# Kernel optimization log

Hardware: AMD Instinct MI355X
Metric: run time of the kernel (lower is better)

Reference implementation:

```python
import jax, jax.numpy as jnp
import numpy as np

N_HEAD = 16


def setup_inputs() -> dict:
    key = jax.random.key(0)
    ks = jax.random.split(key, 9)
    d = 1024
    s = 0.02
    return {
        "x": jax.random.normal(ks[0], (8, 448, d), jnp.float32),
        "xa": jax.random.normal(ks[1], (8, 1500, d), jnp.float32),
        "Wq": jax.random.normal(ks[2], (d, d), jnp.float32) * s,
        "bq": jax.random.normal(ks[3], (d,), jnp.float32) * s,
        "Wk": jax.random.normal(ks[4], (d, d), jnp.float32) * s,
        "Wv": jax.random.normal(ks[5], (d, d), jnp.float32) * s,
        "bv": jax.random.normal(ks[6], (d,), jnp.float32) * s,
        "Wo": jax.random.normal(ks[7], (d, d), jnp.float32) * s,
        "bo": jax.random.normal(ks[8], (d,), jnp.float32) * s,
    }


def reference(x, xa, Wq, bq, Wk, Wv, bv, Wo, bo):
    B, T, D = x.shape
    S = xa.shape[1]
    H = N_HEAD
    Dh = D // H
    scale = Dh ** -0.25  # applied to both q and k, as in the original

    q = x @ Wq + bq            # [B,T,D]
    k = xa @ Wk                # [B,S,D] (no bias)
    v = xa @ Wv + bv           # [B,S,D]

    q = q.reshape(B, T, H, Dh) * scale
    k = k.reshape(B, S, H, Dh) * scale
    v = v.reshape(B, S, H, Dh)

    qk = jnp.einsum("bthd,bshd->bhts", q, k).astype(jnp.float32)  # pre-softmax logits
    w = jax.nn.softmax(qk, axis=-1).astype(q.dtype)
    wv = jnp.einsum("bhts,bshd->bthd", w, v).reshape(B, T, D)

    out = wv @ Wo + bo
    return out, qk
```

## Files before the change

### kernel.cpp

```cpp
#include <hip/hip_runtime.h>
#include <hip/hip_bf16.h>
#include <cstdint>
#include <cstddef>

typedef __bf16  bf16x8  __attribute__((ext_vector_type(8)));
typedef float   f32x4   __attribute__((ext_vector_type(4)));
typedef ushort  ushort8 __attribute__((ext_vector_type(8)));

#define ASYNC16(gp, lp)                                                        \
  __builtin_amdgcn_global_load_lds(                                            \
      (const __attribute__((address_space(1))) void*)(gp),                     \
      (__attribute__((address_space(3))) void*)(lp), 16, 0, 0)

__device__ __forceinline__ ushort f2bf(float f) {
  __hip_bfloat16 h = __float2bfloat16(f);
  ushort u; __builtin_memcpy(&u, &h, 2); return u;
}

#define SINF (-1e30f)

__global__ __launch_bounds__(256) void to_bf16(
    const float* __restrict__ src, ushort* __restrict__ dst, int n8) {
  int i = blockIdx.x * 256 + threadIdx.x;
  const int stride = gridDim.x * 256;
  for (; i < n8; i += stride) {
    const float4* s = (const float4*)(src + (size_t)i * 8);
    float4 a0 = s[0], a1 = s[1];
    ushort8 u = { f2bf(a0.x), f2bf(a0.y), f2bf(a0.z), f2bf(a0.w),
                  f2bf(a1.x), f2bf(a1.y), f2bf(a1.z), f2bf(a1.w) };
    *(ushort8*)&dst[(size_t)i * 8] = u;
  }
}

__global__ __launch_bounds__(256) void transpose_w(
    const float* __restrict__ W0, const float* __restrict__ W1,
    const float* __restrict__ W2, const float* __restrict__ W3,
    ushort* __restrict__ out) {
  __shared__ float tile[32][33];
  const float* W = blockIdx.z == 0 ? W0 : blockIdx.z == 1 ? W1
                 : blockIdx.z == 2 ? W2 : W3;
  ushort* T = out + (size_t)blockIdx.z * (1024u * 1024u);
  const int n0 = blockIdx.x * 32, k0 = blockIdx.y * 32;
  const int t = threadIdx.x;
  const int r = t >> 3, c = (t & 7) * 4;
  float4 v = *(const float4*)&W[(size_t)(k0 + r) * 1024 + n0 + c];
  tile[r][c + 0] = v.x; tile[r][c + 1] = v.y;
  tile[r][c + 2] = v.z; tile[r][c + 3] = v.w;
  __syncthreads();
  ushort4 o;
  o.x = f2bf(tile[c + 0][r]); o.y = f2bf(tile[c + 1][r]);
  o.z = f2bf(tile[c + 2][r]); o.w = f2bf(tile[c + 3][r]);
  *(ushort4*)&T[(size_t)(n0 + r) * 1024 + k0 + c] = o;
}

__global__ __launch_bounds__(256) void transpose_v(
    const ushort* __restrict__ v_s, ushort* __restrict__ v_t) {
  __shared__ ushort tile[32][36];
  const int bh = blockIdx.z;
  const int b = bh >> 4, h = bh & 15;
  const int d0 = blockIdx.y * 32;
  const int s0 = blockIdx.x * 32;
  const int t = threadIdx.x;
  const int r = t >> 3, c4 = (t & 7) * 4;
  const int s = s0 + r;
  ushort4 v = {0, 0, 0, 0};
  if (s < 1500)
    v = *(const ushort4*)&v_s[(size_t)(b * 1500 + s) * 1024 + h * 64 + d0 + c4];
  tile[r][c4 + 0] = v.x; tile[r][c4 + 1] = v.y;
  tile[r][c4 + 2] = v.z; tile[r][c4 + 3] = v.w;
  __syncthreads();
  ushort4 o;
  o.x = tile[c4 + 0][r]; o.y = tile[c4 + 1][r];
  o.z = tile[c4 + 2][r]; o.w = tile[c4 + 3][r];
  *(ushort4*)&v_t[((size_t)bh * 64 + d0 + r) * 1536 + s0 + c4] = o;
}

template <bool A_F32, bool C_F32>
__global__ __launch_bounds__(256) void gemm_bt(
    const void* __restrict__ Ap, const ushort* __restrict__ Bt,
    const float* __restrict__ bias, void* __restrict__ Cp,
    int M, float scale) {
  __shared__ ushort As[128 * 32];
  __shared__ ushort Bs[128 * 32];
  const int tid  = threadIdx.x;
  const int lane = tid & 63, w = tid >> 6;
  const int m15  = lane & 15, q4 = lane >> 4;
  const int wm   = w >> 1,  wn = w & 1;
  const int m0 = blockIdx.x * 128, n0 = blockIdx.y * 128;
  const int sr = lane >> 2;
  const int sc = (lane & 3) * 8;
  f32x4 acc[4][4] = {};
  for (int k0 = 0; k0 < 1024; k0 += 32) {
    __syncthreads();
    #pragma unroll
    for (int j = 0; j < 2; ++j) {
      int n = w * 2 + j;
      int r = n * 16 + sr;
      ASYNC16(&Bt[(size_t)(n0 + r) * 1024 + k0 + sc], &Bs[n * 512]);
    }
    if constexpr (A_F32) {
      const float* Af = (const float*)Ap;
      #pragma unroll
      for (int h = 0; h < 2; ++h) {
        int g = tid + h * 256;
        int row = g >> 2, kg = g & 3;
        int ga = min(m0 + row, M - 1);
        const float* src = &Af[(size_t)ga * 1024 + k0 + kg * 8];
        float4 a0 = *(const float4*)src;
        float4 a1 = *(const float4*)(src + 4);
        ushort8 u = { f2bf(a0.x), f2bf(a0.y), f2bf(a0.z), f2bf(a0.w),
                      f2bf(a1.x), f2bf(a1.y), f2bf(a1.z), f2bf(a1.w) };
        *(ushort8*)&As[row * 32 + kg * 8] = u;
      }
    } else {
      const ushort* Ab = (const ushort*)Ap;
      #pragma unroll
      for (int j = 0; j < 2; ++j) {
        int n = w * 2 + j;
        int r = n * 16 + sr;
        int ga = min(m0 + r, M - 1);
        ASYNC16(&Ab[(size_t)ga * 1024 + k0 + sc], &As[n * 512]);
      }
    }
    __syncthreads();
    bf16x8 af[4], bfr[4];
    #pragma unroll
    for (int i = 0; i < 4; ++i)
      af[i] = *(const bf16x8*)&As[(wm * 64 + i * 16 + m15) * 32 + q4 * 8];
    #pragma unroll
    for (int i = 0; i < 4; ++i)
      bfr[i] = *(const bf16x8*)&Bs[(wn * 64 + i * 16 + m15) * 32 + q4 * 8];
    #pragma unroll
    for (int i = 0; i < 4; ++i)
      #pragma unroll
      for (int j = 0; j < 4; ++j)
        acc[i][j] = __builtin_amdgcn_mfma_f32_16x16x32_bf16(af[i], bfr[j],
                                                            acc[i][j], 0, 0, 0);
  }
  #pragma unroll
  for (int j = 0; j < 4; ++j) {
    int col = n0 + wn * 64 + j * 16 + m15;
    float bb = bias ? bias[col] : 0.f;
    #pragma unroll
    for (int i = 0; i < 4; ++i) {
      #pragma unroll
      for (int r = 0; r < 4; ++r) {
        int row = m0 + wm * 64 + i * 16 + q4 * 4 + r;
        if (row < M) {
          float v = (acc[i][j][r] + bb) * scale;
          if constexpr (C_F32)
            ((float*)Cp)[(size_t)row * 1024 + col] = v;
          else
            ((ushort*)Cp)[(size_t)row * 1024 + col] = f2bf(v);
        }
      }
    }
  }
}

__global__ __launch_bounds__(256) void attn(
    const ushort* __restrict__ q_s, const ushort* __restrict__ k_s,
    const ushort* __restrict__ v_t, float* __restrict__ qk_out,
    ushort* __restrict__ wv) {
  __shared__ ushort Kb[64 * 64];
  __shared__ ushort Pw[4][16 * 72];
  const int tid  = threadIdx.x;
  const int lane = tid & 63, w = tid >> 6;
  const int m15  = lane & 15, q4 = lane >> 4;
  const int h = blockIdx.y, b = blockIdx.z;
  const int t0 = blockIdx.x * 64;
  const int trow = t0 + w * 16;
  const ushort* qrow = &q_s[(size_t)(b * 448 + trow + m15) * 1024 + h * 64];
  bf16x8 qf0 = *(const bf16x8*)&qrow[q4 * 8];
  bf16x8 qf1 = *(const bf16x8*)&qrow[32 + q4 * 8];
  f32x4 o[4] = {};
  float m_r[4] = {SINF, SINF, SINF, SINF};
  float l_r[4] = {0.f, 0.f, 0.f, 0.f};
  const int krb = lane >> 3;
  const int kc_sw = (((lane & 7) ^ krb) * 8);
  const ushort* vbase =
      &v_t[((size_t)(b * 16 + h) * 64 + m15) * 1536 + q4 * 8];
  for (int s0 = 0; s0 < 1500; s0 += 64) {
    __syncthreads();
    #pragma unroll
    for (int j = 0; j < 2; ++j) {
      int n = w * 2 + j;
      int sg = min(s0 + n * 8 + krb, 1499);
      ASYNC16(&k_s[(size_t)(b * 1500 + sg) * 1024 + h * 64 + kc_sw],
              &Kb[n * 512]);
    }
    __syncthreads();
    f32x4 lg[4];
    #pragma unroll
    for (int scol = 0; scol < 4; ++scol) {
      const int r = scol * 16 + m15;
      const int sw = (m15 & 7) * 8;
      bf16x8 kf0 = *(const bf16x8*)&Kb[r * 64 + ((q4 * 8) ^ sw)];
      bf16x8 kf1 = *(const bf16x8*)&Kb[r * 64 + ((32 + q4 * 8) ^ sw)];
      f32x4 a = {};
      a = __builtin_amdgcn_mfma_f32_16x16x32_bf16(qf0, kf0, a, 0, 0, 0);
      a = __builtin_amdgcn_mfma_f32_16x16x32_bf16(qf1, kf1, a, 0, 0, 0);
      lg[scol] = a;
    }
    float mc[4] = {SINF, SINF, SINF, SINF};
    #pragma unroll
    for (int scol = 0; scol < 4; ++scol) {
      bool valid = (s0 + scol * 16 + m15) < 1500;
      #pragma unroll
      for (int r = 0; r < 4; ++r)
        mc[r] = fmaxf(mc[r], valid ? lg[scol][r] : SINF);
    }
    #pragma unroll
    for (int off = 1; off < 16; off <<= 1)
      #pragma unroll
      for (int r = 0; r < 4; ++r)
        mc[r] = fmaxf(mc[r], __shfl_xor(mc[r], off));
    #pragma unroll
    for (int r = 0; r < 4; ++r) {
      float mn = fmaxf(m_r[r], mc[r]);
      float alpha = __expf(m_r[r] - mn);
      l_r[r] *= alpha;
      #pragma unroll
      for (int d = 0; d < 4; ++d) o[d][r] *= alpha;
      m_r[r] = mn;
    }
    float psum[4] = {0.f, 0.f, 0.f, 0.f};
    #pragma unroll
    for (int scol = 0; scol < 4; ++scol) {
      int sg = s0 + scol * 16 + m15;
      bool valid = sg < 1500;
      #pragma unroll
      for (int r = 0; r < 4; ++r) {
        float lv = lg[scol][r];
        float p = valid ? __expf(lv - m_r[r]) : 0.f;
        psum[r] += p;
        Pw[w][(q4 * 4 + r) * 72 + scol * 16 + m15] = f2bf(p);
        if (valid)
          qk_out[(size_t)((b * 16 + h) * 448 + trow + q4 * 4 + r) * 1500 + sg]
              = lv;
      }
    }
    #pragma unroll
    for (int off = 1; off < 16; off <<= 1)
      #pragma unroll
      for (int r = 0; r < 4; ++r)
        psum[r] += __shfl_xor(psum[r], off);
    #pragma unroll
    for (int r = 0; r < 4; ++r) l_r[r] += psum[r];
    #pragma unroll
    for (int ks = 0; ks < 2; ++ks) {
      bf16x8 vf[4];
      #pragma unroll
      for (int d = 0; d < 4; ++d)
        vf[d] = *(const bf16x8*)&vbase[(size_t)(d * 16) * 1536 + s0 + ks * 32];
      bf16x8 pf = *(const bf16x8*)&Pw[w][m15 * 72 + ks * 32 + q4 * 8];
      #pragma unroll
      for (int d = 0; d < 4; ++d)
        o[d] = __builtin_amdgcn_mfma_f32_16x16x32_bf16(pf, vf[d], o[d], 0, 0, 0);
    }
  }
  #pragma unroll
  for (int d = 0; d < 4; ++d)
    #pragma unroll
    for (int r = 0; r < 4; ++r) {
      float val = o[d][r] / l_r[r];
      wv[(size_t)(b * 448 + trow + q4 * 4 + r) * 1024 + h * 64 + d * 16 + m15]
          = f2bf(val);
    }
}

extern "C" void kernel_launch(void* const* d_in, const int* in_sizes, int n_in,
                              void* d_out, int out_size, void* d_ws,
                              size_t ws_size, hipStream_t stream) {
  const float* x  = (const float*)d_in[0];
  const float* xa = (const float*)d_in[1];
  const float* Wq = (const float*)d_in[2];
  const float* bq = (const float*)d_in[3];
  const float* Wk = (const float*)d_in[4];
  const float* Wv = (const float*)d_in[5];
  const float* bv = (const float*)d_in[6];
  const float* Wo = (const float*)d_in[7];
  const float* bo = (const float*)d_in[8];
  float* out = (float*)d_out;
  float* qk  = out + (size_t)8 * 448 * 1024;
  char* ws = (char*)d_ws;
  ushort* Wt    = (ushort*)ws;
  ushort* q_s   = (ushort*)(ws + (size_t)8   * 1024 * 1024);
  ushort* k_s   = (ushort*)(ws + (size_t)16  * 1024 * 1024);
  ushort* v_s   = (ushort*)(ws + (size_t)42  * 1024 * 1024);
  ushort* wv_s  = (ushort*)(ws + (size_t)68  * 1024 * 1024);
  ushort* x_bf  = (ushort*)(ws + (size_t)76  * 1024 * 1024);
  ushort* xa_bf = (ushort*)(ws + (size_t)84  * 1024 * 1024);
  ushort* v_t   = (ushort*)(ws + (size_t)112 * 1024 * 1024);

  to_bf16<<<dim3(1792), 256, 0, stream>>>(x,  x_bf,  458752);
  to_bf16<<<dim3(2048), 256, 0, stream>>>(xa, xa_bf, 1536000);
  transpose_w<<<dim3(32, 32, 4), 256, 0, stream>>>(Wq, Wk, Wv, Wo, Wt);
  const float sc = 0.35355339059327373f;
  gemm_bt<false, false><<<dim3(28, 8), 256, 0, stream>>>(x_bf,  Wt,               bq,      q_s, 3584,  sc);
  gemm_bt<false, false><<<dim3(94, 8), 256, 0, stream>>>(xa_bf, Wt + 1u*1048576u, nullptr, k_s, 12000, sc);
  gemm_bt<false, false><<<dim3(94, 8), 256, 0, stream>>>(xa_bf, Wt + 2u*1048576u, bv,      v_s, 12000, 1.0f);
  transpose_v<<<dim3(48, 2, 128), 256, 0, stream>>>(v_s, v_t);
  attn<<<dim3(7, 16, 8), 256, 0, stream>>>(q_s, k_s, v_t, qk, wv_s);
  gemm_bt<false, true ><<<dim3(28, 8), 256, 0, stream>>>(wv_s, Wt + 3u*1048576u, bo,      out, 3584,  1.0f);
}
```

Baseline: 737.6 us.

## Double-buffer K tiles in attention, fuse K/V GEMMs, convert x inside Q GEMM

The attention kernel processes 128-key tiles with double-buffered async K loads, prefetching the next tile while computing the current one. It also pads the transposed V stride to 1600 so tail reads stay in bounds, and writes logits with nontemporal stores. The K and V projections are merged into one launch, and the Q projection converts fp32 x on the fly, removing a separate conversion kernel. LDS use per block grows and may lower occupancy, and the prefetch correctness depends on the wait inserted before the buffer is reused.

```diff
diff --git a/kernel.cpp b/kernel.cpp
--- a/kernel.cpp
+++ b/kernel.cpp
@@ -72,7 +72,7 @@
   ushort4 o;
   o.x = tile[c4 + 0][r]; o.y = tile[c4 + 1][r];
   o.z = tile[c4 + 2][r]; o.w = tile[c4 + 3][r];
-  *(ushort4*)&v_t[((size_t)bh * 64 + d0 + r) * 1536 + s0 + c4] = o;
+  *(ushort4*)&v_t[((size_t)bh * 64 + d0 + r) * 1600 + s0 + c4] = o;
 }
 
 template <bool A_F32, bool C_F32>
@@ -101,8 +101,8 @@
     if constexpr (A_F32) {
       const float* Af = (const float*)Ap;
       #pragma unroll
-      for (int h = 0; h < 2; ++h) {
-        int g = tid + h * 256;
+      for (int hh = 0; hh < 2; ++hh) {
+        int g = tid + hh * 256;
         int row = g >> 2, kg = g & 3;
         int ga = min(m0 + row, M - 1);
         const float* src = &Af[(size_t)ga * 1024 + k0 + kg * 8];
@@ -158,18 +158,81 @@
   }
 }
 
+__global__ __launch_bounds__(256) void gemm_kv(
+    const ushort* __restrict__ Ab, const ushort* __restrict__ Bt,
+    const float* __restrict__ bv, ushort* __restrict__ k_s,
+    ushort* __restrict__ v_s, int M, float sck) {
+  __shared__ ushort As[128 * 32];
+  __shared__ ushort Bs[128 * 32];
+  const int tid  = threadIdx.x;
+  const int lane = tid & 63, w = tid >> 6;
+  const int m15  = lane & 15, q4 = lane >> 4;
+  const int wm   = w >> 1,  wn = w & 1;
+  const int m0 = blockIdx.x * 128, n0 = blockIdx.y * 128;
+  const int sr = lane >> 2;
+  const int sc = (lane & 3) * 8;
+  f32x4 acc[4][4] = {};
+  for (int k0 = 0; k0 < 1024; k0 += 32) {
+    __syncthreads();
+    #pragma unroll
+    for (int j = 0; j < 2; ++j) {
+      int n = w * 2 + j;
+      int r = n * 16 + sr;
+      ASYNC16(&Bt[(size_t)(n0 + r) * 1024 + k0 + sc], &Bs[n * 512]);
+    }
+    #pragma unroll
+    for (int j = 0; j < 2; ++j) {
+      int n = w * 2 + j;
+      int r = n * 16 + sr;
+      int ga = min(m0 + r, M - 1);
+      ASYNC16(&Ab[(size_t)ga * 1024 + k0 + sc], &As[n * 512]);
+    }
+    __syncthreads();
+    bf16x8 af[4], bfr[4];
+    #pragma unroll
+    for (int i = 0; i < 4; ++i)
+      af[i] = *(const bf16x8*)&As[(wm * 64 + i * 16 + m15) * 32 + q4 * 8];
+    #pragma unroll
+    for (int i = 0; i < 4; ++i)
+      bfr[i] = *(const bf16x8*)&Bs[(wn * 64 + i * 16 + m15) * 32 + q4 * 8];
+    #pragma unroll
+    for (int i = 0; i < 4; ++i)
+      #pragma unroll
+      for (int j = 0; j < 4; ++j)
+        acc[i][j] = __builtin_amdgcn_mfma_f32_16x16x32_bf16(af[i], bfr[j],
+                                                            acc[i][j], 0, 0, 0);
+  }
+  const bool isv = n0 >= 1024;
+  ushort* C = isv ? v_s : k_s;
+  const int nb = isv ? n0 - 1024 : n0;
+  const float scale = isv ? 1.0f : sck;
+  #pragma unroll
+  for (int j = 0; j < 4; ++j) {
+    int col = nb + wn * 64 + j * 16 + m15;
+    float bb = isv ? bv[col] : 0.f;
+    #pragma unroll
+    for (int i = 0; i < 4; ++i) {
+      #pragma unroll
+      for (int r = 0; r < 4; ++r) {
+        int row = m0 + wm * 64 + i * 16 + q4 * 4 + r;
+        if (row < M)
+          C[(size_t)row * 1024 + col] = f2bf((acc[i][j][r] + bb) * scale);
+      }
+    }
+  }
+}
+
 __global__ __launch_bounds__(256) void attn(
     const ushort* __restrict__ q_s, const ushort* __restrict__ k_s,
     const ushort* __restrict__ v_t, float* __restrict__ qk_out,
     ushort* __restrict__ wv) {
-  __shared__ ushort Kb[64 * 64];
-  __shared__ ushort Pw[4][16 * 72];
+  __shared__ ushort Kb[2 * 128 * 64];
+  __shared__ ushort Pw[4][16 * 136];
   const int tid  = threadIdx.x;
   const int lane = tid & 63, w = tid >> 6;
   const int m15  = lane & 15, q4 = lane >> 4;
   const int h = blockIdx.y, b = blockIdx.z;
-  const int t0 = blockIdx.x * 64;
-  const int trow = t0 + w * 16;
+  const int trow = blockIdx.x * 64 + w * 16;
   const ushort* qrow = &q_s[(size_t)(b * 448 + trow + m15) * 1024 + h * 64];
   bf16x8 qf0 = *(const bf16x8*)&qrow[q4 * 8];
   bf16x8 qf1 = *(const bf16x8*)&qrow[32 + q4 * 8];
@@ -177,26 +240,39 @@
   float m_r[4] = {SINF, SINF, SINF, SINF};
   float l_r[4] = {0.f, 0.f, 0.f, 0.f};
   const int krb = lane >> 3;
-  const int kc_sw = (((lane & 7) ^ krb) * 8);
-  const ushort* vbase =
-      &v_t[((size_t)(b * 16 + h) * 64 + m15) * 1536 + q4 * 8];
-  for (int s0 = 0; s0 < 1500; s0 += 64) {
-    __syncthreads();
-    #pragma unroll
-    for (int j = 0; j < 2; ++j) {
-      int n = w * 2 + j;
-      int sg = min(s0 + n * 8 + krb, 1499);
-      ASYNC16(&k_s[(size_t)(b * 1500 + sg) * 1024 + h * 64 + kc_sw],
-              &Kb[n * 512]);
-    }
-    __syncthreads();
-    f32x4 lg[4];
-    #pragma unroll
-    for (int scol = 0; scol < 4; ++scol) {
+  const int kc_sw = ((lane & 7) ^ krb) * 8;
+  const ushort* kbase = &k_s[(size_t)(b * 1500) * 1024 + h * 64 + kc_sw];
+  const ushort* vbase = &v_t[((size_t)(b * 16 + h) * 64 + m15) * 1600 + q4 * 8];
+
+  #pragma unroll
+  for (int j = 0; j < 4; ++j) {
+    int n = w * 4 + j;
+    int sg = min(n * 8 + krb, 1499);
+    ASYNC16(&kbase[(size_t)sg * 1024], &Kb[n * 512]);
+  }
+  __syncthreads();
+
+  for (int t = 0; t < 12; ++t) {
+    const int s0 = t * 128;
+    const ushort* Kc = &Kb[(t & 1) * (128 * 64)];
+    if (t + 1 < 12) {
+      __builtin_amdgcn_sched_barrier(0);
+      ushort* Kn = (ushort*)&Kb[((t + 1) & 1) * (128 * 64)];
+      #pragma unroll
+      for (int j = 0; j < 4; ++j) {
+        int n = w * 4 + j;
+        int sg = min(s0 + 128 + n * 8 + krb, 1499);
+        ASYNC16(&kbase[(size_t)sg * 1024], &Kn[n * 512]);
+      }
+      __builtin_amdgcn_sched_barrier(0);
+    }
+    f32x4 lg[8];
+    #pragma unroll
+    for (int scol = 0; scol < 8; ++scol) {
       const int r = scol * 16 + m15;
       const int sw = (m15 & 7) * 8;
-      bf16x8 kf0 = *(const bf16x8*)&Kb[r * 64 + ((q4 * 8) ^ sw)];
-      bf16x8 kf1 = *(const bf16x8*)&Kb[r * 64 + ((32 + q4 * 8) ^ sw)];
+      bf16x8 kf0 = *(const bf16x8*)&Kc[r * 64 + ((q4 * 8) ^ sw)];
+      bf16x8 kf1 = *(const bf16x8*)&Kc[r * 64 + ((32 + q4 * 8) ^ sw)];
       f32x4 a = {};
       a = __builtin_amdgcn_mfma_f32_16x16x32_bf16(qf0, kf0, a, 0, 0, 0);
       a = __builtin_amdgcn_mfma_f32_16x16x32_bf16(qf1, kf1, a, 0, 0, 0);
@@ -204,7 +280,7 @@
     }
     float mc[4] = {SINF, SINF, SINF, SINF};
     #pragma unroll
-    for (int scol = 0; scol < 4; ++scol) {
+    for (int scol = 0; scol < 8; ++scol) {
       bool valid = (s0 + scol * 16 + m15) < 1500;
       #pragma unroll
       for (int r = 0; r < 4; ++r)
@@ -226,7 +302,7 @@
     }
     float psum[4] = {0.f, 0.f, 0.f, 0.f};
     #pragma unroll
-    for (int scol = 0; scol < 4; ++scol) {
+    for (int scol = 0; scol < 8; ++scol) {
       int sg = s0 + scol * 16 + m15;
       bool valid = sg < 1500;
       #pragma unroll
@@ -234,10 +310,11 @@
         float lv = lg[scol][r];
         float p = valid ? __expf(lv - m_r[r]) : 0.f;
         psum[r] += p;
-        Pw[w][(q4 * 4 + r) * 72 + scol * 16 + m15] = f2bf(p);
+        Pw[w][(q4 * 4 + r) * 136 + scol * 16 + m15] = f2bf(p);
         if (valid)
-          qk_out[(size_t)((b * 16 + h) * 448 + trow + q4 * 4 + r) * 1500 + sg]
-              = lv;
+          __builtin_nontemporal_store(
+              lv, &qk_out[(size_t)((b * 16 + h) * 448 + trow + q4 * 4 + r)
+                              * 1500 + sg]);
       }
     }
     #pragma unroll
@@ -248,16 +325,19 @@
     #pragma unroll
     for (int r = 0; r < 4; ++r) l_r[r] += psum[r];
     #pragma unroll
-    for (int ks = 0; ks < 2; ++ks) {
+    for (int ks = 0; ks < 4; ++ks) {
       bf16x8 vf[4];
       #pragma unroll
       for (int d = 0; d < 4; ++d)
-        vf[d] = *(const bf16x8*)&vbase[(size_t)(d * 16) * 1536 + s0 + ks * 32];
-      bf16x8 pf = *(const bf16x8*)&Pw[w][m15 * 72 + ks * 32 + q4 * 8];
+        vf[d] = *(const bf16x8*)&vbase[(size_t)(d * 16) * 1600 + s0 + ks * 32];
+      bf16x8 pf = *(const bf16x8*)&Pw[w][m15 * 136 + ks * 32 + q4 * 8];
       #pragma unroll
       for (int d = 0; d < 4; ++d)
         o[d] = __builtin_amdgcn_mfma_f32_16x16x32_bf16(pf, vf[d], o[d], 0, 0, 0);
     }
+    __builtin_amdgcn_sched_barrier(0);
+    __builtin_amdgcn_s_barrier();
+    __builtin_amdgcn_sched_barrier(0);
   }
   #pragma unroll
   for (int d = 0; d < 4; ++d)
@@ -289,18 +369,17 @@
   ushort* k_s   = (ushort*)(ws + (size_t)16  * 1024 * 1024);
   ushort* v_s   = (ushort*)(ws + (size_t)42  * 1024 * 1024);
   ushort* wv_s  = (ushort*)(ws + (size_t)68  * 1024 * 1024);
-  ushort* x_bf  = (ushort*)(ws + (size_t)76  * 1024 * 1024);
   ushort* xa_bf = (ushort*)(ws + (size_t)84  * 1024 * 1024);
   ushort* v_t   = (ushort*)(ws + (size_t)112 * 1024 * 1024);
 
-  to_bf16<<<dim3(1792), 256, 0, stream>>>(x,  x_bf,  458752);
   to_bf16<<<dim3(2048), 256, 0, stream>>>(xa, xa_bf, 1536000);
   transpose_w<<<dim3(32, 32, 4), 256, 0, stream>>>(Wq, Wk, Wv, Wo, Wt);
   const float sc = 0.35355339059327373f;
-  gemm_bt<false, false><<<dim3(28, 8), 256, 0, stream>>>(x_bf,  Wt,               bq,      q_s, 3584,  sc);
-  gemm_bt<false, false><<<dim3(94, 8), 256, 0, stream>>>(xa_bf, Wt + 1u*1048576u, nullptr, k_s, 12000, sc);
-  gemm_bt<false, false><<<dim3(94, 8), 256, 0, stream>>>(xa_bf, Wt + 2u*1048576u, bv,      v_s, 12000, 1.0f);
-  transpose_v<<<dim3(48, 2, 128), 256, 0, stream>>>(v_s, v_t);
+  gemm_bt<true, false><<<dim3(28, 8), 256, 0, stream>>>(x, Wt, bq, q_s, 3584, sc);
+  gemm_kv<<<dim3(94, 16), 256, 0, stream>>>(xa_bf, Wt + 1u * 1048576u, bv,
+                                            k_s, v_s, 12000, sc);
+  transpose_v<<<dim3(50, 2, 128), 256, 0, stream>>>(v_s, v_t);
   attn<<<dim3(7, 16, 8), 256, 0, stream>>>(q_s, k_s, v_t, qk, wv_s);
-  gemm_bt<false, true ><<<dim3(28, 8), 256, 0, stream>>>(wv_s, Wt + 3u*1048576u, bo,      out, 3584,  1.0f);
-}
+  gemm_bt<false, true><<<dim3(28, 8), 256, 0, stream>>>(wv_s, Wt + 3u * 1048576u,
+                                                        bo, out, 3584, 1.0f);
+}
```

After: 718.5 us. 2.6% less time.
